# Kernel tuning notes

Measured on AMD Instinct MI355X. Metric: run time of the kernel, lower is better.

The kernel has to match this reference:

```python
import jax, jax.numpy as jnp
import numpy as np
from jax import lax

NEGINF = -100000.0
START_IDX = 0  # y_codebook['__START__']
TAGSET = 16


def setup_inputs() -> dict:
    key = jax.random.key(0)
    ks = jax.random.split(key, 8)
    D, H, K, T = 1024, 1024, TAGSET, 8192
    seq = jax.random.normal(ks[0], (1, T, D), dtype=jnp.float32)
    # PyTorch-layout LSTM params: gates ordered (i, f, g, o)
    s = 1.0 / np.sqrt(H)
    W_ih = jax.random.uniform(ks[1], (4 * H, D), jnp.float32, -s, s)
    W_hh = jax.random.uniform(ks[2], (4 * H, H), jnp.float32, -s, s)
    b_ih = jax.random.uniform(ks[3], (4 * H,), jnp.float32, -s, s)
    b_hh = jax.random.uniform(ks[4], (4 * H,), jnp.float32, -s, s)
    W_tag = jax.random.uniform(ks[5], (K, H), jnp.float32, -s, s)
    b_tag = jax.random.uniform(ks[6], (K,), jnp.float32, -s, s)
    trans = jax.random.normal(ks[7], (K, K), dtype=jnp.float32)
    trans = trans.at[:, START_IDX].set(NEGINF)  # nothing transitions INTO start
    return {"seq": seq, "W_ih": W_ih, "W_hh": W_hh, "b_ih": b_ih,
            "b_hh": b_hh, "W_tag": W_tag, "b_tag": b_tag, "trans": trans}


def _lstm(x, W_ih, W_hh, b_ih, b_hh):
    # x: (T, D) -> hidden states (T, H); PyTorch gate order i,f,g,o
    H = W_hh.shape[1]
    x_gates = x @ W_ih.T + (b_ih + b_hh)  # (T, 4H) precomputed input part

    def step(carry, gx):
        h, c = carry
        g = gx + h @ W_hh.T
        i, f, gg, o = jnp.split(g, 4)
        i, f, o = jax.nn.sigmoid(i), jax.nn.sigmoid(f), jax.nn.sigmoid(o)
        c = f * c + i * jnp.tanh(gg)
        h = o * jnp.tanh(c)
        return (h, c), h

    init = (jnp.zeros((H,), x.dtype), jnp.zeros((H,), x.dtype))
    _, hs = lax.scan(step, init, x_gates)
    return hs  # (T, H)


def reference(seq, W_ih, W_hh, b_ih, b_hh, W_tag, b_tag, trans):
    # --- compute_potential (batch=1) ---
    x = seq[0]                                  # (T, D)
    rnnout = _lstm(x, W_ih, W_hh, b_ih, b_hh)    # (T, H)
    feat = rnnout @ W_tag.T + b_tag              # (T, K) unary potentials

    # --- compute_forward_vec: alpha recursion in log-semiring ---
    # feat_score[t, i, j] = feat[t, j] + trans[i, j]
    feat_score = feat[:, None, :] + trans[None, :, :]  # (T, K, K)
    K = trans.shape[0]
    alpha0 = jnp.full((K,), NEGINF, dtype=feat.dtype).at[START_IDX].set(0.0)

    def step(a, fs):
        a_new = jax.nn.logsumexp(a[:, None] + fs, axis=0)  # (K,)
        return a_new, a_new

    a_T, rows = lax.scan(step, alpha0, feat_score)
    alpha = jnp.concatenate([alpha0[None, :], rows], axis=0)  # (T+1, K)
    Z = jax.nn.logsumexp(a_T)  # log partition (no stop state)
    return Z, alpha
```

## Files before the change

### kernel.cpp

```cpp
#include <hip/hip_runtime.h>
#include <hip/hip_bf16.h>
#include <math.h>

#define T_LEN   8192
#define D_IN    1024
#define H_DIM   1024
#define G4      4096
#define K_TAG   16
#define NWG     128
#define NC      128
#define CLEN    64
#define NEGINF_V (-100000.0f)

__global__ void k_init(const float* __restrict__ b_ih, const float* __restrict__ b_hh,
                       float* __restrict__ bsum, float* __restrict__ h0,
                       unsigned long long* __restrict__ htag) {
  int tid = blockIdx.x * 256 + threadIdx.x;
  if (tid < G4) bsum[tid] = b_ih[tid] + b_hh[tid];
  if (tid < H_DIM) h0[tid] = 0.f;
  if (tid < 2 * H_DIM) htag[tid] = 0ULL;
}

__global__ __launch_bounds__(256) void k_gemm_xg(
    const float* __restrict__ A,
    const float* __restrict__ B,
    const float* __restrict__ bsum,
    __hip_bfloat16* __restrict__ xg)
{
  __shared__ __align__(16) float As[16][132];
  __shared__ __align__(16) float Bs[16][132];
  const int tid = threadIdx.x;
  const int n0 = blockIdx.x * 128;
  const int m0 = blockIdx.y * 128;
  const int ty = tid >> 4, tx = tid & 15;
  float acc[8][8] = {};

  for (int k0 = 0; k0 < D_IN; k0 += 16) {
#pragma unroll
    for (int p0 = 0; p0 < 2; ++p0) {
      int p = tid + p0 * 256;
      int row = p >> 2;
      int c4 = (p & 3) * 4;
      float4 va = *(const float4*)&A[(size_t)(m0 + row) * D_IN + k0 + c4];
      As[c4 + 0][row] = va.x; As[c4 + 1][row] = va.y;
      As[c4 + 2][row] = va.z; As[c4 + 3][row] = va.w;
      float4 vb = *(const float4*)&B[(size_t)(n0 + row) * D_IN + k0 + c4];
      Bs[c4 + 0][row] = vb.x; Bs[c4 + 1][row] = vb.y;
      Bs[c4 + 2][row] = vb.z; Bs[c4 + 3][row] = vb.w;
    }
    __syncthreads();
#pragma unroll
    for (int k = 0; k < 16; ++k) {
      float4 a0 = *(const float4*)&As[k][ty * 8];
      float4 a1 = *(const float4*)&As[k][ty * 8 + 4];
      float4 b0 = *(const float4*)&Bs[k][tx * 8];
      float4 b1 = *(const float4*)&Bs[k][tx * 8 + 4];
      float av[8] = {a0.x, a0.y, a0.z, a0.w, a1.x, a1.y, a1.z, a1.w};
      float bv[8] = {b0.x, b0.y, b0.z, b0.w, b1.x, b1.y, b1.z, b1.w};
#pragma unroll
      for (int i = 0; i < 8; ++i)
#pragma unroll
        for (int j = 0; j < 8; ++j)
          acc[i][j] = fmaf(av[i], bv[j], acc[i][j]);
    }
    __syncthreads();
  }

#pragma unroll
  for (int i = 0; i < 8; ++i) {
    size_t m = (size_t)(m0 + ty * 8 + i);
    union { __hip_bfloat16 h[8]; uint4 v; } pk;
#pragma unroll
    for (int j = 0; j < 8; ++j)
      pk.h[j] = __float2bfloat16(acc[i][j] + bsum[n0 + tx * 8 + j]);
    *(uint4*)&xg[m * G4 + n0 + tx * 8] = pk.v;
  }
}

__global__ __launch_bounds__(256) void k_lstm(
    const float* __restrict__ W_hh,
    const __hip_bfloat16* __restrict__ xg,
    float* __restrict__ h_all,
    unsigned long long* __restrict__ htag)
{
  __shared__ __align__(16) float h_lds[H_DIM];
  __shared__ float gates[32];
  __shared__ float c_sl[8];

  const int tid = threadIdx.x;
  const int w = blockIdx.x;
  const int rl = tid >> 3;
  const int sub = tid & 7;
  const int q = rl >> 3, r = rl & 7;
  const int grow = q * H_DIM + w * 8 + r;
  const int e = tid * 4;

  float4 w4[32];
#pragma unroll
  for (int k = 0; k < 32; ++k)
    w4[k] = *(const float4*)&W_hh[(size_t)grow * H_DIM + sub * 4 + 32 * k];

  if (tid < 8) c_sl[tid] = 0.f;
  __syncthreads();

  for (int t = 1; t <= T_LEN; ++t) {
    float xgv = 0.f;
    if (sub == 0)
      xgv = __bfloat162float(xg[(size_t)(t - 1) * G4 + grow]);

    unsigned long long* hb = htag + (((t - 1) & 1) << 10);
    const unsigned tgt = (unsigned)(t - 1);
    unsigned long long x0, x1, x2, x3;
    for (;;) {
      x0 = __hip_atomic_load(hb + e + 0, __ATOMIC_RELAXED, __HIP_MEMORY_SCOPE_AGENT);
      x1 = __hip_atomic_load(hb + e + 1, __ATOMIC_RELAXED, __HIP_MEMORY_SCOPE_AGENT);
      x2 = __hip_atomic_load(hb + e + 2, __ATOMIC_RELAXED, __HIP_MEMORY_SCOPE_AGENT);
      x3 = __hip_atomic_load(hb + e + 3, __ATOMIC_RELAXED, __HIP_MEMORY_SCOPE_AGENT);
      unsigned t0 = (unsigned)(x0 >> 32), t1 = (unsigned)(x1 >> 32);
      unsigned t2 = (unsigned)(x2 >> 32), t3 = (unsigned)(x3 >> 32);
      unsigned mn = min(min(t0, t1), min(t2, t3));
      if (mn >= tgt) break;
      __builtin_amdgcn_s_sleep(1);
    }
    h_lds[e + 0] = __uint_as_float((unsigned)x0);
    h_lds[e + 1] = __uint_as_float((unsigned)x1);
    h_lds[e + 2] = __uint_as_float((unsigned)x2);
    h_lds[e + 3] = __uint_as_float((unsigned)x3);
    __syncthreads();

    float acc = 0.f;
#pragma unroll
    for (int k = 0; k < 32; ++k) {
      float4 hv = ((const float4*)h_lds)[sub + 8 * k];
      acc = fmaf(w4[k].x, hv.x, acc);
      acc = fmaf(w4[k].y, hv.y, acc);
      acc = fmaf(w4[k].z, hv.z, acc);
      acc = fmaf(w4[k].w, hv.w, acc);
    }
    acc += __shfl_xor(acc, 1);
    acc += __shfl_xor(acc, 2);
    acc += __shfl_xor(acc, 4);
    if (sub == 0)
      gates[rl] = acc + xgv;
    __syncthreads();

    if (tid < 8) {
      float gi = gates[tid],      gf = gates[8 + tid];
      float gg = gates[16 + tid], go = gates[24 + tid];
      float si = 1.f / (1.f + expf(-gi));
      float sf = 1.f / (1.f + expf(-gf));
      float so = 1.f / (1.f + expf(-go));
      float c = sf * c_sl[tid] + si * tanhf(gg);
      c_sl[tid] = c;
      float h = so * tanhf(c);
      h_all[(size_t)t * H_DIM + w * 8 + tid] = h;
      unsigned long long pk = ((unsigned long long)(unsigned)t << 32) |
                              (unsigned long long)__float_as_uint(h);
      __hip_atomic_store(htag + ((t & 1) << 10) + w * 8 + tid, pk,
                         __ATOMIC_RELAXED, __HIP_MEMORY_SCOPE_AGENT);
    }
  }
}

__device__ __forceinline__ float lse16(float v) {
  float m = v;
  m = fmaxf(m, __shfl_xor(m, 1));
  m = fmaxf(m, __shfl_xor(m, 2));
  m = fmaxf(m, __shfl_xor(m, 4));
  m = fmaxf(m, __shfl_xor(m, 8));
  float e = expf(v - m);
  e += __shfl_xor(e, 1);
  e += __shfl_xor(e, 2);
  e += __shfl_xor(e, 4);
  e += __shfl_xor(e, 8);
  return m + logf(e);
}

__global__ __launch_bounds__(256) void k_chunk(
    const float* __restrict__ h_all,
    const float* __restrict__ W_tag, const float* __restrict__ b_tag,
    const float* __restrict__ trans,
    float* __restrict__ featbuf,
    float* __restrict__ Pbuf)
{
  __shared__ float trs[16][17];
  __shared__ float featc[CLEN][16];
  __shared__ __align__(16) float hrow[H_DIM];
  __shared__ float red[16][17];
  __shared__ float Pa[16][17], Pb[16][17];

  const int tid = threadIdx.x;
  const int c = blockIdx.x;
  trs[tid >> 4][tid & 15] = trans[tid];

  const int jj = tid & 15, part = tid >> 4;
  for (int u = 0; u < CLEN; ++u) {
    int s = c * CLEN + 1 + u;
    ((float4*)hrow)[tid] = ((const float4*)(h_all + (size_t)s * H_DIM))[tid];
    __syncthreads();
    const float* wt = W_tag + (size_t)jj * H_DIM + part * 64;
    const float* hp = hrow + part * 64;
    float4 a4 = {0.f, 0.f, 0.f, 0.f};
#pragma unroll
    for (int k2 = 0; k2 < 64; k2 += 4) {
      float4 hv = *(const float4*)(hp + k2);
      float4 wv = *(const float4*)(wt + k2);
      a4.x = fmaf(hv.x, wv.x, a4.x);
      a4.y = fmaf(hv.y, wv.y, a4.y);
      a4.z = fmaf(hv.z, wv.z, a4.z);
      a4.w = fmaf(hv.w, wv.w, a4.w);
    }
    red[jj][part] = (a4.x + a4.y) + (a4.z + a4.w);
    __syncthreads();
    if (tid < 16) {
      float ssum = b_tag[tid];
#pragma unroll
      for (int pp = 0; pp < 16; ++pp) ssum += red[tid][pp];
      featc[u][tid] = ssum;
      featbuf[(size_t)s * K_TAG + tid] = ssum;
    }
    __syncthreads();
  }

  const int i = tid >> 4, j = tid & 15;
  Pa[i][j] = trs[i][j] + featc[0][j];
  __syncthreads();
  float* Pr = &Pa[0][0];
  float* Pw = &Pb[0][0];
  for (int u = 1; u < CLEN; ++u) {
    float fj = featc[u][j];
    float m = -3.0e38f;
#pragma unroll
    for (int k = 0; k < 16; ++k) m = fmaxf(m, Pr[i * 17 + k] + trs[k][j]);
    float e = 0.f;
#pragma unroll
    for (int k = 0; k < 16; ++k) e += expf(Pr[i * 17 + k] + trs[k][j] - m);
    Pw[i * 17 + j] = m + fj + logf(e);
    __syncthreads();
    float* tsw = Pr; Pr = Pw; Pw = tsw;
  }
  Pbuf[(size_t)c * 256 + i * 16 + j] = Pr[i * 17 + j];
}

__global__ __launch_bounds__(256) void k_scan(
    const float* __restrict__ Pbuf,
    float* __restrict__ bbuf,
    float* __restrict__ out)
{
  __shared__ float Pl[16][17];
  __shared__ float bcur[16], bnew[16];
  const int tid = threadIdx.x;
  const int i = tid & 15, j = tid >> 4;
  if (tid < 16) {
    float a0 = (tid == 0) ? 0.f : NEGINF_V;
    bcur[tid] = a0;
    bbuf[tid] = a0;
    out[1 + tid] = a0;
  }
  __syncthreads();
  for (int c = 0; c < NC; ++c) {
    Pl[tid >> 4][tid & 15] = Pbuf[(size_t)c * 256 + tid];
    __syncthreads();
    float r_ = lse16(bcur[i] + Pl[i][j]);
    if (i == 0) bnew[j] = r_;
    __syncthreads();
    if (tid < 16) {
      bcur[tid] = bnew[tid];
      bbuf[(size_t)(c + 1) * K_TAG + tid] = bnew[tid];
    }
    __syncthreads();
  }
  if (tid < 16) {
    float z = lse16(bcur[tid]);
    if (tid == 0) out[0] = z;
  }
}

__global__ __launch_bounds__(256) void k_alpha(
    const float* __restrict__ featbuf, const float* __restrict__ trans,
    const float* __restrict__ bbuf, float* __restrict__ out)
{
  __shared__ float trs[16][17];
  __shared__ float acur[16], anew[16];
  const int tid = threadIdx.x;
  const int c = blockIdx.x;
  trs[tid >> 4][tid & 15] = trans[tid];
  if (tid < 16) acur[tid] = bbuf[(size_t)c * K_TAG + tid];
  __syncthreads();
  const int i = tid & 15, j = tid >> 4;
  for (int u = 0; u < CLEN; ++u) {
    int s = c * CLEN + 1 + u;
    float v = acur[i] + trs[i][j] + featbuf[(size_t)s * K_TAG + j];
    float r_ = lse16(v);
    if (i == 0) anew[j] = r_;
    __syncthreads();
    if (tid < 16) {
      acur[tid] = anew[tid];
      out[1 + (size_t)s * K_TAG + tid] = anew[tid];
    }
    __syncthreads();
  }
}

extern "C" void kernel_launch(void* const* d_in, const int* in_sizes, int n_in,
                              void* d_out, int out_size, void* d_ws, size_t ws_size,
                              hipStream_t stream) {
  (void)in_sizes; (void)n_in; (void)out_size; (void)ws_size;
  const float* seq   = (const float*)d_in[0];
  const float* W_ih  = (const float*)d_in[1];
  const float* W_hh  = (const float*)d_in[2];
  const float* b_ih  = (const float*)d_in[3];
  const float* b_hh  = (const float*)d_in[4];
  const float* W_tag = (const float*)d_in[5];
  const float* b_tag = (const float*)d_in[6];
  const float* trans = (const float*)d_in[7];
  float* out = (float*)d_out;

  char* base = (char*)d_ws;
  size_t off = 0;
  auto take = [&](size_t nbytes) -> void* {
    void* p = base + off;
    off += (nbytes + 255) & ~(size_t)255;
    return p;
  };
  __hip_bfloat16* xg = (__hip_bfloat16*)take((size_t)T_LEN * G4 * sizeof(__hip_bfloat16));
  float* h_all   = (float*)take((size_t)(T_LEN + 1) * H_DIM * sizeof(float));
  float* featbuf = (float*)take((size_t)(T_LEN + 1) * K_TAG * sizeof(float));
  float* Pbuf    = (float*)take((size_t)NC * 256 * sizeof(float));
  float* bbuf    = (float*)take((size_t)(NC + 1) * K_TAG * sizeof(float));
  float* bsum    = (float*)take((size_t)G4 * sizeof(float));
  unsigned long long* htag = (unsigned long long*)take((size_t)2 * H_DIM * sizeof(unsigned long long));

  k_init<<<16, 256, 0, stream>>>(b_ih, b_hh, bsum, h_all, htag);
  k_gemm_xg<<<dim3(G4 / 128, T_LEN / 128), 256, 0, stream>>>(seq, W_ih, bsum, xg);
  k_lstm<<<NWG, 256, 0, stream>>>(W_hh, xg, h_all, htag);
  k_chunk<<<NC, 256, 0, stream>>>(h_all, W_tag, b_tag, trans, featbuf, Pbuf);
  k_scan<<<1, 256, 0, stream>>>(Pbuf, bbuf, out);
  k_alpha<<<NC, 256, 0, stream>>>(featbuf, trans, bbuf, out);
}
```

Baseline: 23.31 ms.

## Keep LSTM gate math in-wave with shuffles and double-buffer h in LDS

Each wavefront now owns all four gates for two hidden units, so the gate combine uses wave shuffles instead of an LDS gates array and a second __syncthreads per step. The cell state lives in registers, and h is double-buffered in LDS so only one barrier per timestep is needed. The global h polling loads are made coalesced (strided by tid) and the s_sleep in the spin loop is removed. Together these target per-step latency in the serial recurrence, at the cost of more aggressive polling traffic on the flag array.

```diff
diff --git a/kernel.cpp b/kernel.cpp
--- a/kernel.cpp
+++ b/kernel.cpp
@@ -83,55 +83,53 @@
     float* __restrict__ h_all,
     unsigned long long* __restrict__ htag)
 {
-  __shared__ __align__(16) float h_lds[H_DIM];
-  __shared__ float gates[32];
-  __shared__ float c_sl[8];
+  __shared__ __align__(16) float h_lds[2][H_DIM];
 
   const int tid = threadIdx.x;
   const int w = blockIdx.x;
-  const int rl = tid >> 3;
-  const int sub = tid & 7;
-  const int q = rl >> 3, r = rl & 7;
-  const int grow = q * H_DIM + w * 8 + r;
-  const int e = tid * 4;
+  const int lane = tid & 63;
+  const int v = tid >> 6;
+  const int rl8 = lane >> 3;
+  const int sub = lane & 7;
+  const int g = rl8 >> 1, b = rl8 & 1;
+  const int j = 2 * v + b;
+  const int grow = g * H_DIM + w * 8 + j;
 
   float4 w4[32];
 #pragma unroll
   for (int k = 0; k < 32; ++k)
     w4[k] = *(const float4*)&W_hh[(size_t)grow * H_DIM + sub * 4 + 32 * k];
 
-  if (tid < 8) c_sl[tid] = 0.f;
-  __syncthreads();
+  float c_reg = 0.f;
 
   for (int t = 1; t <= T_LEN; ++t) {
-    float xgv = 0.f;
-    if (sub == 0)
-      xgv = __bfloat162float(xg[(size_t)(t - 1) * G4 + grow]);
+    float xgv = __bfloat162float(xg[(size_t)(t - 1) * G4 + grow]);
 
     unsigned long long* hb = htag + (((t - 1) & 1) << 10);
     const unsigned tgt = (unsigned)(t - 1);
     unsigned long long x0, x1, x2, x3;
     for (;;) {
-      x0 = __hip_atomic_load(hb + e + 0, __ATOMIC_RELAXED, __HIP_MEMORY_SCOPE_AGENT);
-      x1 = __hip_atomic_load(hb + e + 1, __ATOMIC_RELAXED, __HIP_MEMORY_SCOPE_AGENT);
-      x2 = __hip_atomic_load(hb + e + 2, __ATOMIC_RELAXED, __HIP_MEMORY_SCOPE_AGENT);
-      x3 = __hip_atomic_load(hb + e + 3, __ATOMIC_RELAXED, __HIP_MEMORY_SCOPE_AGENT);
+      x0 = __hip_atomic_load(hb + tid,       __ATOMIC_RELAXED, __HIP_MEMORY_SCOPE_AGENT);
+      x1 = __hip_atomic_load(hb + tid + 256, __ATOMIC_RELAXED, __HIP_MEMORY_SCOPE_AGENT);
+      x2 = __hip_atomic_load(hb + tid + 512, __ATOMIC_RELAXED, __HIP_MEMORY_SCOPE_AGENT);
+      x3 = __hip_atomic_load(hb + tid + 768, __ATOMIC_RELAXED, __HIP_MEMORY_SCOPE_AGENT);
       unsigned t0 = (unsigned)(x0 >> 32), t1 = (unsigned)(x1 >> 32);
       unsigned t2 = (unsigned)(x2 >> 32), t3 = (unsigned)(x3 >> 32);
       unsigned mn = min(min(t0, t1), min(t2, t3));
       if (mn >= tgt) break;
-      __builtin_amdgcn_s_sleep(1);
-    }
-    h_lds[e + 0] = __uint_as_float((unsigned)x0);
-    h_lds[e + 1] = __uint_as_float((unsigned)x1);
-    h_lds[e + 2] = __uint_as_float((unsigned)x2);
-    h_lds[e + 3] = __uint_as_float((unsigned)x3);
-    __syncthreads();
-
+    }
+    float* hl = h_lds[(t - 1) & 1];
+    hl[tid      ] = __uint_as_float((unsigned)x0);
+    hl[tid + 256] = __uint_as_float((unsigned)x1);
+    hl[tid + 512] = __uint_as_float((unsigned)x2);
+    hl[tid + 768] = __uint_as_float((unsigned)x3);
+    __syncthreads();
+
+    const float4* h4 = (const float4*)hl;
     float acc = 0.f;
 #pragma unroll
     for (int k = 0; k < 32; ++k) {
-      float4 hv = ((const float4*)h_lds)[sub + 8 * k];
+      float4 hv = h4[sub + 8 * k];
       acc = fmaf(w4[k].x, hv.x, acc);
       acc = fmaf(w4[k].y, hv.y, acc);
       acc = fmaf(w4[k].z, hv.z, acc);
@@ -140,23 +138,25 @@
     acc += __shfl_xor(acc, 1);
     acc += __shfl_xor(acc, 2);
     acc += __shfl_xor(acc, 4);
-    if (sub == 0)
-      gates[rl] = acc + xgv;
-    __syncthreads();
-
-    if (tid < 8) {
-      float gi = gates[tid],      gf = gates[8 + tid];
-      float gg = gates[16 + tid], go = gates[24 + tid];
+    acc += xgv;
+
+    const int bl = lane & 8;
+    float gi = __shfl(acc, bl);
+    float gf = __shfl(acc, bl | 16);
+    float gg = __shfl(acc, bl | 32);
+    float go = __shfl(acc, bl | 48);
+
+    if ((lane & 55) == 0) {
       float si = 1.f / (1.f + expf(-gi));
       float sf = 1.f / (1.f + expf(-gf));
       float so = 1.f / (1.f + expf(-go));
-      float c = sf * c_sl[tid] + si * tanhf(gg);
-      c_sl[tid] = c;
-      float h = so * tanhf(c);
-      h_all[(size_t)t * H_DIM + w * 8 + tid] = h;
+      c_reg = sf * c_reg + si * tanhf(gg);
+      float h = so * tanhf(c_reg);
+      const int hidx = w * 8 + j;
+      h_all[(size_t)t * H_DIM + hidx] = h;
       unsigned long long pk = ((unsigned long long)(unsigned)t << 32) |
                               (unsigned long long)__float_as_uint(h);
-      __hip_atomic_store(htag + ((t & 1) << 10) + w * 8 + tid, pk,
+      __hip_atomic_store(htag + ((t & 1) << 10) + hidx, pk,
                          __ATOMIC_RELAXED, __HIP_MEMORY_SCOPE_AGENT);
     }
   }
```

New measurement: 30.01 ms. 1.29x slower.
